# Optimization experiments

Hardware: AMD Instinct MI355X
Metric: run time of the kernel (lower is better)

Reference implementation:

```python
import jax, jax.numpy as jnp
import numpy as np

N_NODES = 50000
N_EDGES = 800000
N_GRAPHS = 512
EPS = 1e-5
SLOPE = 0.2  # LeakyReLU negative slope in GATv2


def setup_inputs() -> dict:
    key = jax.random.key(0)
    ks = jax.random.split(key, 20)
    s = 0.1
    inp = {
        "x": jax.random.normal(ks[0], (N_NODES, 9), jnp.float32),
        "edge_attr": jax.random.normal(ks[1], (N_EDGES, 3), jnp.float32),
        "Wl0": jax.random.normal(ks[2], (9, 64), jnp.float32) * s,
        "Wr0": jax.random.normal(ks[3], (9, 64), jnp.float32) * s,
        "bl0": jnp.zeros((64,), jnp.float32),
        "br0": jnp.zeros((64,), jnp.float32),
        "We0": jax.random.normal(ks[4], (3, 64), jnp.float32) * s,
        "att0": jax.random.normal(ks[5], (64,), jnp.float32) * s,
        "bo0": jnp.zeros((64,), jnp.float32),
        "Wl": jax.random.normal(ks[6], (4, 64, 64), jnp.float32) * s,
        "Wr": jax.random.normal(ks[7], (4, 64, 64), jnp.float32) * s,
        "bl": jnp.zeros((4, 64), jnp.float32),
        "br": jnp.zeros((4, 64), jnp.float32),
        "We": jax.random.normal(ks[8], (4, 3, 64), jnp.float32) * s,
        "att": jax.random.normal(ks[9], (4, 64), jnp.float32) * s,
        "bo": jnp.zeros((4, 64), jnp.float32),
        "bn_g": jnp.ones((5, 64), jnp.float32),
        "bn_b": jnp.zeros((5, 64), jnp.float32),
        "bn_m": jnp.zeros((5, 64), jnp.float32),
        "bn_v": jax.random.uniform(ks[10], (5, 64), jnp.float32, 0.5, 1.5),
        "Wjk": jax.random.normal(ks[11], (64, 64), jnp.float32) * s,
        "bjk": jnp.zeros((64,), jnp.float32),
        "Whead": jax.random.normal(ks[12], (64, 1), jnp.float32) * s,
        "bhead": jnp.zeros((1,), jnp.float32),
        "edge_index": jax.random.randint(ks[13], (2, N_EDGES), 0, N_NODES, jnp.int32),
        "batch": jnp.sort(jax.random.randint(ks[14], (N_NODES,), 0, N_GRAPHS, jnp.int32)),
        "num_graphs": N_GRAPHS,
    }
    return inp


def gatv2_layer(h, src, dst, ea, Wl_, bl_, Wr_, br_, We_, a_, bo_, n_nodes):
    # GATv2Conv (heads=1, edge_dim) : e_ij = a . LeakyReLU(Wl h_j + Wr h_i + We e_ij)
    xl = h @ Wl_ + bl_                          # [N, 64] source transform
    xr = h @ Wr_ + br_                          # [N, 64] dest transform
    e = jax.nn.leaky_relu(xl[src] + xr[dst] + ea @ We_, SLOPE)  # [E, 64]
    logit = e @ a_                              # [E]
    m = jax.ops.segment_max(logit, dst, num_segments=n_nodes)
    m = jnp.where(jnp.isfinite(m), m, 0.0)      # empty segments -> -inf
    p = jnp.exp(logit - m[dst])
    z = jax.ops.segment_sum(p, dst, num_segments=n_nodes)
    alpha = p / jnp.maximum(z[dst], 1e-16)      # softmax over in-edges of dst
    out = jax.ops.segment_sum(alpha[:, None] * xl[src], dst, num_segments=n_nodes)
    return out + bo_


def bn_relu(h, g, b, m, v):
    # eval-mode BatchNorm1d followed by ReLU (BasicGNN: norm then act)
    return jax.nn.relu((h - m) * (g * jax.lax.rsqrt(v + EPS)) + b)


def reference(x, edge_attr, Wl0, Wr0, bl0, br0, We0, att0, bo0,
              Wl, Wr, bl, br, We, att, bo,
              bn_g, bn_b, bn_m, bn_v, Wjk, bjk, Whead, bhead,
              edge_index, batch, num_graphs):
    n = x.shape[0]
    src, dst = edge_index[0], edge_index[1]
    h = gatv2_layer(x, src, dst, edge_attr, Wl0, bl0, Wr0, br0, We0, att0, bo0, n)
    h = bn_relu(h, bn_g[0], bn_b[0], bn_m[0], bn_v[0])
    for i in range(4):
        h = gatv2_layer(h, src, dst, edge_attr, Wl[i], bl[i], Wr[i], br[i], We[i], att[i], bo[i], n)
        h = bn_relu(h, bn_g[i + 1], bn_b[i + 1], bn_m[i + 1], bn_v[i + 1])
    h = h @ Wjk + bjk                            # jk='last' output projection 64->64
    # global mean pool over graphs
    sums = jax.ops.segment_sum(h, batch, num_segments=num_graphs)          # [G, 64]
    cnt = jax.ops.segment_sum(jnp.ones((n,), h.dtype), batch, num_segments=num_graphs)
    pooled = sums / jnp.maximum(cnt, 1.0)[:, None]
    return pooled @ Whead + bhead                # [G, 1]  (dropout inactive in eval)
```

## Files before the change

kernel.cpp:

```cpp
#include <hip/hip_runtime.h>
#include <math.h>

#define N_NODES 50000
#define N_EDGES 800000
#define N_GRAPHS 512
#define SLOPE 0.2f
#define CAP 48
static constexpr float EPS_BN = 1e-5f;

typedef float v2f __attribute__((ext_vector_type(2)));


__global__ __launch_bounds__(256) void scatter_t9_kernel(
    const int* __restrict__ src, const int* __restrict__ dst,
    const float* __restrict__ ea,
    int* __restrict__ cnt, float4* __restrict__ rec,
    const float* __restrict__ x,
    const float* __restrict__ Wl0, const float* __restrict__ bl0,
    const float* __restrict__ Wr0, const float* __restrict__ br0,
    float* __restrict__ xl, float* __restrict__ xr) {
    int t = threadIdx.x;
    int e = blockIdx.x * 256 + t;
    if (e < N_EDGES) {
        int d = dst[e];
        int pos = atomicAdd(&cnt[d], 1);
        if (pos < CAP)
            rec[(size_t)d * CAP + pos] = make_float4(__int_as_float(src[e] * 64),
                                                     ea[e * 3 + 0], ea[e * 3 + 1], ea[e * 3 + 2]);
    }

    int w = t >> 6;
    int k = t & 63;
    v2f wlr[9];
#pragma unroll
    for (int j = 0; j < 9; j++) wlr[j] = (v2f){Wl0[j * 64 + k], Wr0[j * 64 + k]};
    v2f bias = {bl0[k], br0[k]};
    const int NW = gridDim.x * 4;
    for (int n = blockIdx.x * 4 + w; n < N_NODES; n += NW) {
        int un = __builtin_amdgcn_readfirstlane(n);
        const float* __restrict__ hrow = x + (size_t)un * 9;
        float hb[9];
#pragma unroll
        for (int j = 0; j < 9; j++) hb[j] = hrow[j];
        v2f acc = bias;
#pragma unroll
        for (int j = 0; j < 9; j++)
            acc = __builtin_elementwise_fma((v2f){hb[j], hb[j]}, wlr[j], acc);
        xl[(size_t)un * 64 + k] = acc.x;
        xr[(size_t)un * 64 + k] = acc.y;
    }
}


__global__ __launch_bounds__(256) void transform6_kernel(
    const float* __restrict__ h,
    const float* __restrict__ Wl, const float* __restrict__ bl,
    const float* __restrict__ Wr, const float* __restrict__ br,
    float* __restrict__ xl, float* __restrict__ xr) {
    __shared__ float sAt[64][68];
    __shared__ float sB[64][128];
    int t = threadIdx.x;
    int n0 = blockIdx.x * 64;

#pragma unroll
    for (int i = 0; i < 4; i++) {
        int idx = i * 256 + t;
        int row = idx >> 4;
        int fc  = idx & 15;
        int n = n0 + row;
        float4 v = (n < N_NODES) ? *((const float4*)(h + (size_t)n * 64 + fc * 4))
                                 : make_float4(0.f, 0.f, 0.f, 0.f);
        sAt[fc * 4 + 0][row] = v.x;
        sAt[fc * 4 + 1][row] = v.y;
        sAt[fc * 4 + 2][row] = v.z;
        sAt[fc * 4 + 3][row] = v.w;
    }
#pragma unroll
    for (int i = 0; i < 8; i++) {
        int idx = i * 256 + t;
        int j  = idx >> 5;
        int fc = idx & 31;
        int c  = fc * 4;
        float4 v = (c < 64) ? *((const float4*)(Wl + j * 64 + c))
                            : *((const float4*)(Wr + j * 64 + (c - 64)));
        *((float4*)&sB[j][c]) = v;
    }
    __syncthreads();

    int tx = t & 15, ty = t >> 4;
    int c0 = tx * 4;
    float4 bls = *((const float4*)(bl + c0));
    float4 brs = *((const float4*)(br + c0));
    v2f acc[4][4];
#pragma unroll
    for (int r = 0; r < 4; r++) {
        acc[r][0] = (v2f){bls.x, bls.y};
        acc[r][1] = (v2f){bls.z, bls.w};
        acc[r][2] = (v2f){brs.x, brs.y};
        acc[r][3] = (v2f){brs.z, brs.w};
    }

#pragma unroll 4
    for (int j = 0; j < 64; j++) {
        float a0 = sAt[j][ty * 4 + 0];
        float a1 = sAt[j][ty * 4 + 1];
        float a2 = sAt[j][ty * 4 + 2];
        float a3 = sAt[j][ty * 4 + 3];
        float4 bq0 = *((const float4*)&sB[j][c0]);
        float4 bq1 = *((const float4*)&sB[j][64 + c0]);
        v2f b0 = {bq0.x, bq0.y}, b1 = {bq0.z, bq0.w};
        v2f b2 = {bq1.x, bq1.y}, b3 = {bq1.z, bq1.w};
        v2f a0v = {a0, a0}, a1v = {a1, a1}, a2v = {a2, a2}, a3v = {a3, a3};
        acc[0][0] = __builtin_elementwise_fma(a0v, b0, acc[0][0]);
        acc[0][1] = __builtin_elementwise_fma(a0v, b1, acc[0][1]);
        acc[0][2] = __builtin_elementwise_fma(a0v, b2, acc[0][2]);
        acc[0][3] = __builtin_elementwise_fma(a0v, b3, acc[0][3]);
        acc[1][0] = __builtin_elementwise_fma(a1v, b0, acc[1][0]);
        acc[1][1] = __builtin_elementwise_fma(a1v, b1, acc[1][1]);
        acc[1][2] = __builtin_elementwise_fma(a1v, b2, acc[1][2]);
        acc[1][3] = __builtin_elementwise_fma(a1v, b3, acc[1][3]);
        acc[2][0] = __builtin_elementwise_fma(a2v, b0, acc[2][0]);
        acc[2][1] = __builtin_elementwise_fma(a2v, b1, acc[2][1]);
        acc[2][2] = __builtin_elementwise_fma(a2v, b2, acc[2][2]);
        acc[2][3] = __builtin_elementwise_fma(a2v, b3, acc[2][3]);
        acc[3][0] = __builtin_elementwise_fma(a3v, b0, acc[3][0]);
        acc[3][1] = __builtin_elementwise_fma(a3v, b1, acc[3][1]);
        acc[3][2] = __builtin_elementwise_fma(a3v, b2, acc[3][2]);
        acc[3][3] = __builtin_elementwise_fma(a3v, b3, acc[3][3]);
    }

#pragma unroll
    for (int r = 0; r < 4; r++) {
        int n = n0 + ty * 4 + r;
        if (n < N_NODES) {
            *((float4*)(xl + (size_t)n * 64 + c0)) =
                make_float4(acc[r][0].x, acc[r][0].y, acc[r][1].x, acc[r][1].y);
            *((float4*)(xr + (size_t)n * 64 + c0)) =
                make_float4(acc[r][2].x, acc[r][2].y, acc[r][3].x, acc[r][3].y);
        }
    }
}


#define EDGE_T(rX, xXa, xXb, accX)                                        \
    {                                                                     \
        v2f tXa = xXa + xra, tXb = xXb + xrb;                             \
        tXa = __builtin_elementwise_fma((v2f){rX.y, rX.y}, we0a, tXa);    \
        tXb = __builtin_elementwise_fma((v2f){rX.y, rX.y}, we0b, tXb);    \
        tXa = __builtin_elementwise_fma((v2f){rX.z, rX.z}, we1a, tXa);    \
        tXb = __builtin_elementwise_fma((v2f){rX.z, rX.z}, we1b, tXb);    \
        tXa = __builtin_elementwise_fma((v2f){rX.w, rX.w}, we2a, tXa);    \
        tXb = __builtin_elementwise_fma((v2f){rX.w, rX.w}, we2b, tXb);    \
        tXa = __builtin_elementwise_max(tXa, tXa * SLOPE);                \
        tXb = __builtin_elementwise_max(tXb, tXb * SLOPE);                \
        v2f dX = ata * tXa;                                               \
        dX = __builtin_elementwise_fma(atb, tXb, dX);                     \
        accX = dX.x + dX.y;                                               \
    }

__global__ __launch_bounds__(256) void gat_fused9_kernel(
    const float* __restrict__ xl, const float* __restrict__ xr,
    const float4* __restrict__ recP, const int* __restrict__ cnt,
    const float* __restrict__ We, const float* __restrict__ att,
    const float* __restrict__ bo,
    const float* __restrict__ bn_g, const float* __restrict__ bn_b,
    const float* __restrict__ bn_m, const float* __restrict__ bn_v,
    float* __restrict__ hout) {
    int t = threadIdx.x;
    int w = t >> 6;
    int lane = t & 63;
    int q = lane >> 4;
    int r = lane & 15;
    int k4 = r * 4;

    float4 we0 = *(const float4*)(We + 0 * 64 + k4);
    float4 we1 = *(const float4*)(We + 64 + k4);
    float4 we2 = *(const float4*)(We + 128 + k4);
    float4 at4 = *(const float4*)(att + k4);
    v2f we0a = {we0.x, we0.y}, we0b = {we0.z, we0.w};
    v2f we1a = {we1.x, we1.y}, we1b = {we1.z, we1.w};
    v2f we2a = {we2.x, we2.y}, we2b = {we2.z, we2.w};
    v2f ata  = {at4.x, at4.y}, atb  = {at4.z, at4.w};
    float4 bo4 = *(const float4*)(bo + k4);
    float4 g4  = *(const float4*)(bn_g + k4);
    float4 b4  = *(const float4*)(bn_b + k4);
    float4 m4  = *(const float4*)(bn_m + k4);
    float4 v4  = *(const float4*)(bn_v + k4);
    float4 S, C;
    S.x = g4.x / sqrtf(v4.x + EPS_BN);  C.x = (bo4.x - m4.x) * S.x + b4.x;
    S.y = g4.y / sqrtf(v4.y + EPS_BN);  C.y = (bo4.y - m4.y) * S.y + b4.y;
    S.z = g4.z / sqrtf(v4.z + EPS_BN);  C.z = (bo4.z - m4.z) * S.z + b4.z;
    S.w = g4.w / sqrtf(v4.w + EPS_BN);  C.w = (bo4.w - m4.w) * S.w + b4.w;

    const int NW = gridDim.x * 4;
    for (int n0 = blockIdx.x * 4 + w; n0 < N_NODES; n0 += NW) {
        int n = __builtin_amdgcn_readfirstlane(n0);
        float4 xq = *(const float4*)(xr + (size_t)n * 64 + k4);
        v2f xra = {xq.x, xq.y}, xrb = {xq.z, xq.w};
        int beg = n * CAP;
        int end = beg + min(cnt[n], CAP);

        v2f oAa = {0.f, 0.f}, oAb = {0.f, 0.f};
        v2f oBa = {0.f, 0.f}, oBb = {0.f, 0.f};
        float zA = 0.f, zB = 0.f;

        int c = beg;
        int pA = c + q;     bool vA = pA < end;
        int pB = c + 4 + q; bool vB = pB < end;
        float4 rA = recP[vA ? pA : beg];
        float4 rB = recP[vB ? pB : beg];

        while (c < end) {
            unsigned offA = (unsigned)__float_as_int(rA.x) + k4;
            unsigned offB = (unsigned)__float_as_int(rB.x) + k4;
            float4 xA = *(const float4*)(xl + offA);
            float4 xB = *(const float4*)(xl + offB);

            int c2 = c + 8;
            int pA2 = c2 + q;     bool vA2 = pA2 < end;
            int pB2 = c2 + 4 + q; bool vB2 = pB2 < end;
            float4 rA2 = recP[vA2 ? pA2 : beg];
            float4 rB2 = recP[vB2 ? pB2 : beg];

            v2f xAa = {xA.x, xA.y}, xAb = {xA.z, xA.w};
            v2f xBa = {xB.x, xB.y}, xBb = {xB.z, xB.w};

            float accA, accB;
            EDGE_T(rA, xAa, xAb, accA);
            EDGE_T(rB, xBa, xBb, accB);

            accA += __shfl_xor(accA, 1, 64);  accB += __shfl_xor(accB, 1, 64);
            accA += __shfl_xor(accA, 2, 64);  accB += __shfl_xor(accB, 2, 64);
            accA += __shfl_xor(accA, 4, 64);  accB += __shfl_xor(accB, 4, 64);
            accA += __shfl_xor(accA, 8, 64);  accB += __shfl_xor(accB, 8, 64);

            float peA = vA ? __expf(accA) : 0.f;
            float peB = vB ? __expf(accB) : 0.f;
            v2f pA2v = {peA, peA}, pB2v = {peB, peB};
            oAa = __builtin_elementwise_fma(pA2v, xAa, oAa);
            oAb = __builtin_elementwise_fma(pA2v, xAb, oAb);
            oBa = __builtin_elementwise_fma(pB2v, xBa, oBa);
            oBb = __builtin_elementwise_fma(pB2v, xBb, oBb);
            zA += peA; zB += peB;

            rA = rA2; rB = rB2; vA = vA2; vB = vB2; c = c2;
        }

        v2f oa = oAa + oBa, ob = oAb + oBb;
        float z = zA + zB;
        float4 o = make_float4(oa.x, oa.y, ob.x, ob.y);
        o.x += __shfl_xor(o.x, 16, 64); o.x += __shfl_xor(o.x, 32, 64);
        o.y += __shfl_xor(o.y, 16, 64); o.y += __shfl_xor(o.y, 32, 64);
        o.z += __shfl_xor(o.z, 16, 64); o.z += __shfl_xor(o.z, 32, 64);
        o.w += __shfl_xor(o.w, 16, 64); o.w += __shfl_xor(o.w, 32, 64);
        z += __shfl_xor(z, 16, 64); z += __shfl_xor(z, 32, 64);

        if (q == 0) {
            float zi = 1.0f / fmaxf(z, 1e-16f);
            float4 res;
            res.x = fmaxf(fmaf(o.x * zi, S.x, C.x), 0.f);
            res.y = fmaxf(fmaf(o.y * zi, S.y, C.y), 0.f);
            res.z = fmaxf(fmaf(o.z * zi, S.z, C.z), 0.f);
            res.w = fmaxf(fmaf(o.w * zi, S.w, C.w), 0.f);
            *(float4*)(hout + (size_t)n * 64 + k4) = res;
        }
    }
}


__global__ __launch_bounds__(256) void pool_all2_kernel(
    const float* __restrict__ h, const int* __restrict__ batch,
    const float* __restrict__ Wjk, const float* __restrict__ bjk,
    const float* __restrict__ Whead, const float* __restrict__ bhead,
    float* __restrict__ out) {
    __shared__ float red[4][64];
    int g = blockIdx.x;
    int t = threadIdx.x;
    int k = t & 63;
    int w = t >> 6;
    int lo = 0, hi = N_NODES;
    while (lo < hi) { int mid = (lo + hi) >> 1; if (batch[mid] < g) lo = mid + 1; else hi = mid; }
    int s = lo;
    hi = N_NODES;
    while (lo < hi) { int mid = (lo + hi) >> 1; if (batch[mid] < g + 1) lo = mid + 1; else hi = mid; }
    int e = lo;

    float acc = 0.f;
    for (int n = s + w; n < e; n += 4) acc += h[(size_t)n * 64 + k];
    red[w][k] = acc;
    __syncthreads();

    if (w == 0) {
        acc = (red[0][k] + red[1][k]) + (red[2][k] + red[3][k]);
        float wc = 0.f;
        for (int j = 0; j < 64; j++) wc = fmaf(Wjk[k * 64 + j], Whead[j], wc);
        float bc = bjk[k] * Whead[k];
        for (int off = 32; off > 0; off >>= 1) bc += __shfl_xor(bc, off, 64);
        float cntf = (float)(e - s);
        acc /= fmaxf(cntf, 1.0f);
        float v = acc * wc;
        for (int off = 32; off > 0; off >>= 1) v += __shfl_xor(v, off, 64);
        if (k == 0) out[g] = v + bc + bhead[0];
    }
}


extern "C" void kernel_launch(void* const* d_in, const int* in_sizes, int n_in,
                              void* d_out, int out_size, void* d_ws, size_t ws_size,
                              hipStream_t stream) {
    const float* x     = (const float*)d_in[0];
    const float* ea    = (const float*)d_in[1];
    const float* Wl0   = (const float*)d_in[2];
    const float* Wr0   = (const float*)d_in[3];
    const float* bl0   = (const float*)d_in[4];
    const float* br0   = (const float*)d_in[5];
    const float* We0   = (const float*)d_in[6];
    const float* att0  = (const float*)d_in[7];
    const float* bo0   = (const float*)d_in[8];
    const float* Wl    = (const float*)d_in[9];
    const float* Wr    = (const float*)d_in[10];
    const float* bl    = (const float*)d_in[11];
    const float* br    = (const float*)d_in[12];
    const float* We    = (const float*)d_in[13];
    const float* att   = (const float*)d_in[14];
    const float* bo    = (const float*)d_in[15];
    const float* bn_g  = (const float*)d_in[16];
    const float* bn_b  = (const float*)d_in[17];
    const float* bn_m  = (const float*)d_in[18];
    const float* bn_v  = (const float*)d_in[19];
    const float* Wjk   = (const float*)d_in[20];
    const float* bjk   = (const float*)d_in[21];
    const float* Whead = (const float*)d_in[22];
    const float* bhead = (const float*)d_in[23];
    const int* edge_index = (const int*)d_in[24];
    const int* batch      = (const int*)d_in[25];

    const int* srcIdx = edge_index;
    const int* dstIdx = edge_index + N_EDGES;

    char* ws = (char*)d_ws;
    size_t off = 0;
    auto alloc = [&](size_t bytes) -> void* {
        void* p = ws + off;
        off += (bytes + 255) & ~(size_t)255;
        return p;
    };
    float* hA      = (float*)alloc((size_t)N_NODES * 64 * 4);
    float* hB      = (float*)alloc((size_t)N_NODES * 64 * 4);
    float* xlb     = (float*)alloc((size_t)N_NODES * 64 * 4);
    float* xrb     = (float*)alloc((size_t)N_NODES * 64 * 4);
    int*   cnt     = (int*)alloc((size_t)N_NODES * 4);
    float4* recP   = (float4*)alloc((size_t)N_NODES * CAP * 16);

    hipMemsetAsync(cnt, 0, (size_t)N_NODES * 4, stream);
    scatter_t9_kernel<<<(N_EDGES + 255) / 256, 256, 0, stream>>>(
        srcIdx, dstIdx, ea, cnt, recP, x, Wl0, bl0, Wr0, br0, xlb, xrb);

    const int GB  = 2048;
    const int NBG = (N_NODES + 63) / 64;

    gat_fused9_kernel<<<GB, 256, 0, stream>>>(xlb, xrb, recP, cnt,
                                              We0, att0, bo0,
                                              bn_g, bn_b, bn_m, bn_v, hA);

    float* hcur = hA;
    float* hnext = hB;
    for (int i = 0; i < 4; i++) {
        transform6_kernel<<<NBG, 256, 0, stream>>>(hcur,
            Wl + (size_t)i * 64 * 64, bl + (size_t)i * 64,
            Wr + (size_t)i * 64 * 64, br + (size_t)i * 64,
            xlb, xrb);
        gat_fused9_kernel<<<GB, 256, 0, stream>>>(xlb, xrb, recP, cnt,
            We + (size_t)i * 3 * 64, att + (size_t)i * 64,
            bo + (size_t)i * 64,
            bn_g + (size_t)(i + 1) * 64, bn_b + (size_t)(i + 1) * 64,
            bn_m + (size_t)(i + 1) * 64, bn_v + (size_t)(i + 1) * 64,
            hnext);
        float* tp = hcur; hcur = hnext; hnext = tp;
    }

    pool_all2_kernel<<<N_GRAPHS, 256, 0, stream>>>(hcur, batch, Wjk, bjk, Whead, bhead,
                                                   (float*)d_out);
}
```

Before: 460.6 us.

## Batch edge scatter per thread, vectorize LDS A loads, prefetch next node in GAT

The scatter kernel now handles four edges per thread, issuing all loads before the atomics so more memory traffic is in flight, and the grid shrinks to match. The transform kernel reads the transposed A tile with a single float4 LDS load instead of four scalar loads. The fused GAT kernel software-pipelines its per-node loop, prefetching the next node's count and xr row while processing the current one, to hide load latency. The trade-offs are higher register pressure and fewer blocks in the scatter kernel, which also reduces parallelism for its fused layer-0 node transform.

```diff
diff --git a/kernel.cpp b/kernel.cpp
--- a/kernel.cpp
+++ b/kernel.cpp
@@ -11,7 +11,7 @@
 typedef float v2f __attribute__((ext_vector_type(2)));
 
 
-__global__ __launch_bounds__(256) void scatter_t9_kernel(
+__global__ __launch_bounds__(256) void scatter_t11_kernel(
     const int* __restrict__ src, const int* __restrict__ dst,
     const float* __restrict__ ea,
     int* __restrict__ cnt, float4* __restrict__ rec,
@@ -20,14 +20,29 @@
     const float* __restrict__ Wr0, const float* __restrict__ br0,
     float* __restrict__ xl, float* __restrict__ xr) {
     int t = threadIdx.x;
-    int e = blockIdx.x * 256 + t;
-    if (e < N_EDGES) {
-        int d = dst[e];
-        int pos = atomicAdd(&cnt[d], 1);
-        if (pos < CAP)
-            rec[(size_t)d * CAP + pos] = make_float4(__int_as_float(src[e] * 64),
-                                                     ea[e * 3 + 0], ea[e * 3 + 1], ea[e * 3 + 2]);
-    }
+    int base = blockIdx.x * 1024 + t;
+    int d[4], s[4], p[4];
+    float a0[4], a1[4], a2[4];
+    bool v[4];
+#pragma unroll
+    for (int i = 0; i < 4; i++) {
+        int e = base + i * 256;
+        v[i] = e < N_EDGES;
+        int ec = v[i] ? e : 0;
+        d[i] = dst[ec];
+        s[i] = src[ec];
+        a0[i] = ea[ec * 3 + 0];
+        a1[i] = ea[ec * 3 + 1];
+        a2[i] = ea[ec * 3 + 2];
+    }
+#pragma unroll
+    for (int i = 0; i < 4; i++)
+        p[i] = v[i] ? atomicAdd(&cnt[d[i]], 1) : CAP;
+#pragma unroll
+    for (int i = 0; i < 4; i++)
+        if (v[i] && p[i] < CAP)
+            rec[(size_t)d[i] * CAP + p[i]] =
+                make_float4(__int_as_float(s[i] * 64), a0[i], a1[i], a2[i]);
 
     int w = t >> 6;
     int k = t & 63;
@@ -52,13 +67,13 @@
 }
 
 
-__global__ __launch_bounds__(256) void transform6_kernel(
+__global__ __launch_bounds__(256) void transform7_kernel(
     const float* __restrict__ h,
     const float* __restrict__ Wl, const float* __restrict__ bl,
     const float* __restrict__ Wr, const float* __restrict__ br,
     float* __restrict__ xl, float* __restrict__ xr) {
-    __shared__ float sAt[64][68];
-    __shared__ float sB[64][128];
+    __shared__ __attribute__((aligned(16))) float sAt[64][68];
+    __shared__ __attribute__((aligned(16))) float sB[64][128];
     int t = threadIdx.x;
     int n0 = blockIdx.x * 64;
 
@@ -102,15 +117,12 @@
 
 #pragma unroll 4
     for (int j = 0; j < 64; j++) {
-        float a0 = sAt[j][ty * 4 + 0];
-        float a1 = sAt[j][ty * 4 + 1];
-        float a2 = sAt[j][ty * 4 + 2];
-        float a3 = sAt[j][ty * 4 + 3];
+        float4 av = *((const float4*)&sAt[j][ty * 4]);
         float4 bq0 = *((const float4*)&sB[j][c0]);
         float4 bq1 = *((const float4*)&sB[j][64 + c0]);
         v2f b0 = {bq0.x, bq0.y}, b1 = {bq0.z, bq0.w};
         v2f b2 = {bq1.x, bq1.y}, b3 = {bq1.z, bq1.w};
-        v2f a0v = {a0, a0}, a1v = {a1, a1}, a2v = {a2, a2}, a3v = {a3, a3};
+        v2f a0v = {av.x, av.x}, a1v = {av.y, av.y}, a2v = {av.z, av.z}, a3v = {av.w, av.w};
         acc[0][0] = __builtin_elementwise_fma(a0v, b0, acc[0][0]);
         acc[0][1] = __builtin_elementwise_fma(a0v, b1, acc[0][1]);
         acc[0][2] = __builtin_elementwise_fma(a0v, b2, acc[0][2]);
@@ -158,7 +170,7 @@
         accX = dX.x + dX.y;                                               \
     }
 
-__global__ __launch_bounds__(256) void gat_fused9_kernel(
+__global__ __launch_bounds__(256) void gat_fused10_kernel(
     const float* __restrict__ xl, const float* __restrict__ xr,
     const float4* __restrict__ recP, const int* __restrict__ cnt,
     const float* __restrict__ We, const float* __restrict__ att,
@@ -193,12 +205,23 @@
     S.w = g4.w / sqrtf(v4.w + EPS_BN);  C.w = (bo4.w - m4.w) * S.w + b4.w;
 
     const int NW = gridDim.x * 4;
-    for (int n0 = blockIdx.x * 4 + w; n0 < N_NODES; n0 += NW) {
-        int n = __builtin_amdgcn_readfirstlane(n0);
-        float4 xq = *(const float4*)(xr + (size_t)n * 64 + k4);
+    int n0 = blockIdx.x * 4 + w;
+    if (n0 >= N_NODES) return;
+    int nU = __builtin_amdgcn_readfirstlane(n0);
+    int cn = cnt[nU];
+    float4 xq = *(const float4*)(xr + (size_t)nU * 64 + k4);
+
+    while (true) {
+        int n = nU;
         v2f xra = {xq.x, xq.y}, xrb = {xq.z, xq.w};
         int beg = n * CAP;
-        int end = beg + min(cnt[n], CAP);
+        int end = beg + min(cn, CAP);
+
+        int n1 = n0 + NW;
+        bool hasNext = n1 < N_NODES;
+        int nU1 = __builtin_amdgcn_readfirstlane(hasNext ? n1 : n0);
+        int cn1 = cnt[nU1];
+        float4 xq1 = *(const float4*)(xr + (size_t)nU1 * 64 + k4);
 
         v2f oAa = {0.f, 0.f}, oAb = {0.f, 0.f};
         v2f oBa = {0.f, 0.f}, oBb = {0.f, 0.f};
@@ -264,6 +287,9 @@
             res.w = fmaxf(fmaf(o.w * zi, S.w, C.w), 0.f);
             *(float4*)(hout + (size_t)n * 64 + k4) = res;
         }
+
+        if (!hasNext) break;
+        n0 = n1; nU = nU1; cn = cn1; xq = xq1;
     }
 }
 
@@ -353,24 +379,25 @@
     float4* recP   = (float4*)alloc((size_t)N_NODES * CAP * 16);
 
     hipMemsetAsync(cnt, 0, (size_t)N_NODES * 4, stream);
-    scatter_t9_kernel<<<(N_EDGES + 255) / 256, 256, 0, stream>>>(
+    const int NSB = (N_EDGES + 1023) / 1024;
+    scatter_t11_kernel<<<NSB, 256, 0, stream>>>(
         srcIdx, dstIdx, ea, cnt, recP, x, Wl0, bl0, Wr0, br0, xlb, xrb);
 
     const int GB  = 2048;
     const int NBG = (N_NODES + 63) / 64;
 
-    gat_fused9_kernel<<<GB, 256, 0, stream>>>(xlb, xrb, recP, cnt,
-                                              We0, att0, bo0,
-                                              bn_g, bn_b, bn_m, bn_v, hA);
+    gat_fused10_kernel<<<GB, 256, 0, stream>>>(xlb, xrb, recP, cnt,
+                                               We0, att0, bo0,
+                                               bn_g, bn_b, bn_m, bn_v, hA);
 
     float* hcur = hA;
     float* hnext = hB;
     for (int i = 0; i < 4; i++) {
-        transform6_kernel<<<NBG, 256, 0, stream>>>(hcur,
+        transform7_kernel<<<NBG, 256, 0, stream>>>(hcur,
             Wl + (size_t)i * 64 * 64, bl + (size_t)i * 64,
             Wr + (size_t)i * 64 * 64, br + (size_t)i * 64,
             xlb, xrb);
-        gat_fused9_kernel<<<GB, 256, 0, stream>>>(xlb, xrb, recP, cnt,
+        gat_fused10_kernel<<<GB, 256, 0, stream>>>(xlb, xrb, recP, cnt,
             We + (size_t)i * 3 * 64, att + (size_t)i * 64,
             bo + (size_t)i * 64,
             bn_g + (size_t)(i + 1) * 64, bn_b + (size_t)(i + 1) * 64,
```

Result: slower. 488.6 us (+6.1%).
